# Performance work log

Measured on AMD Instinct MI355X. Metric: run time of the kernel, lower is better.

## Reference

```python
import jax, jax.numpy as jnp
import numpy as np

DEPTH = 18                     # levels 0..17 of a complete binary tree
N = 2 ** DEPTH - 1             # 262143 nodes, node n's children are 2n+1, 2n+2


def setup_inputs() -> dict:
    key = jax.random.key(0)
    ks = jax.random.split(key, 9)
    V, X, H, C = 32000, 128, 128, 5
    s = 0.05  # weight scale to keep activations in a sane range
    return {
        "x_ids": jax.random.randint(ks[0], (N,), 0, V),
        "mask": jax.random.randint(ks[1], (N,), 0, 2),
        "emb_table": jax.random.normal(ks[2], (V, X), jnp.float32),
        "W_iou": jax.random.normal(ks[3], (X, 3 * H), jnp.float32) * s,
        "U_iou": jax.random.normal(ks[4], (H, 3 * H), jnp.float32) * s,
        "b_iou": jnp.zeros((3 * H,), jnp.float32),
        "W_f": jax.random.normal(ks[5], (X, H), jnp.float32) * s,
        "U_f": jax.random.normal(ks[6], (H, H), jnp.float32) * s,
        "b_f": jnp.zeros((H,), jnp.float32),
        "W_out": jax.random.normal(ks[7], (H, C), jnp.float32) * s,
        "b_out": jnp.zeros((C,), jnp.float32),
    }


def reference(x_ids, mask, emb_table, W_iou, U_iou, b_iou, W_f, U_f, b_f, W_out, b_out):
    H = U_f.shape[0]
    # input_module: embeds = Embedding(x * mask)
    embeds = emb_table[x_ids * mask]                    # [N, X]
    # cell_module.precompute_input_values: per-node input projections
    x_iou = embeds @ W_iou + b_iou                      # [N, 3H]
    x_f = embeds @ W_f + b_f                            # [N, H]

    levels_h = [None] * DEPTH
    levels_c = [None] * DEPTH
    # dgl.prop_nodes_topo: leaves -> root, one synchronized level at a time
    for d in range(DEPTH - 1, -1, -1):
        s0, n = 2 ** d - 1, 2 ** d                      # level-d node range [s0, s0+n)
        iou = x_iou[s0:s0 + n]
        if d < DEPTH - 1:
            # children of level-d node s0+i are contiguous at level d+1: 2i, 2i+1
            h_ch = levels_h[d + 1].reshape(n, 2, H)
            c_ch = levels_c[d + 1].reshape(n, 2, H)
            iou = iou + h_ch.sum(axis=1) @ U_iou        # child-sum of h
            f = jax.nn.sigmoid(x_f[s0:s0 + n][:, None, :] + h_ch @ U_f)  # [n,2,H]
            fc = (f * c_ch).sum(axis=1)
        else:
            fc = jnp.zeros((n, H), iou.dtype)
        i, o, u = jnp.split(iou, 3, axis=-1)
        c = jax.nn.sigmoid(i) * jnp.tanh(u) + fc
        h = jax.nn.sigmoid(o) * jnp.tanh(c)
        levels_h[d] = h
        levels_c[d] = c

    h_all = jnp.concatenate(levels_h, axis=0)           # [N, H], node-index order
    # output_module: per-node linear readout
    return h_all @ W_out + b_out                        # [N, C]
```

## Files before the change

kernel.cpp:

```cpp
#include <hip/hip_runtime.h>

#define DEPTH 18
#define NN ((1 << DEPTH) - 1)

typedef __attribute__((ext_vector_type(8))) short short8;
typedef __attribute__((ext_vector_type(4))) float f32x4;

__device__ __forceinline__ float sigm_(float x) { return 1.f / (1.f + __expf(-x)); }
__device__ __forceinline__ float tanh_(float x) { float e = __expf(2.f * x); return 1.f - 2.f / (e + 1.f); }
__device__ __forceinline__ unsigned short f2bf(float f) {
    union { float f; unsigned int u; } v; v.f = f;
    unsigned int r = (v.u + 0x7fffu + ((v.u >> 16) & 1u)) >> 16;
    return (unsigned short)r;
}
__device__ __forceinline__ float bf2f(unsigned short h) {
    union { unsigned int u; float f; } v; v.u = ((unsigned int)h) << 16; return v.f;
}
__device__ __forceinline__ uint4 bfadd8(uint4 a, uint4 b) {
    const unsigned short* pa = (const unsigned short*)&a;
    const unsigned short* pb = (const unsigned short*)&b;
    uint4 o; unsigned short* po = (unsigned short*)&o;
    #pragma unroll
    for (int i = 0; i < 8; ++i) po[i] = f2bf(bf2f(pa[i]) + bf2f(pb[i]));
    return o;
}

__global__ void cvt_emb(const float* __restrict__ src, unsigned short* __restrict__ dst, int n4) {
    int i = blockIdx.x * 256 + threadIdx.x;
    if (i < n4) {
        float4 v = ((const float4*)src)[i];
        ushort4 o; o.x = f2bf(v.x); o.y = f2bf(v.y); o.z = f2bf(v.z); o.w = f2bf(v.w);
        ((ushort4*)dst)[i] = o;
    }
}

__global__ void build_bpack(const float* __restrict__ Wiou, const float* __restrict__ Uiou,
                            const float* __restrict__ Wf, const float* __restrict__ Uf,
                            unsigned short* __restrict__ pack) {
    int idx = blockIdx.x * 256 + threadIdx.x;
    int c = idx >> 14, r = idx & 16383, j = r >> 5, kl = r & 31;
    int k2 = c * 32 + kl;
    float v;
    if (j < 384) v = (k2 < 128) ? Wiou[k2 * 384 + j] : Uiou[(k2 - 128) * 384 + j];
    else { int jf = j - 384; v = (k2 < 128) ? Wf[k2 * 128 + jf] : Uf[(k2 - 128) * 128 + jf]; }
    pack[idx] = f2bf(v);
}

__global__ void build_woutT(const float* __restrict__ Wout, float* __restrict__ woutT) {
    int i = blockIdx.x * 256 + threadIdx.x;
    if (i < 640) { int c = i >> 7, k = i & 127; woutT[c * 132 + k] = Wout[k * 5 + c]; }
}

template<int HC>
__global__ __launch_bounds__(256, 2) void tree_level_mfma(
    const int* __restrict__ xids, const int* __restrict__ msk,
    const unsigned short* __restrict__ embB, const unsigned short* __restrict__ bpack,
    const float* __restrict__ biou, const float* __restrict__ bfv,
    const float* __restrict__ woutT, const float* __restrict__ bout,
    unsigned short* __restrict__ hB, float* __restrict__ c_ws, float* __restrict__ outp,
    int s0)
{
    __shared__ __align__(16) unsigned short A_s[16896];

    const int t  = threadIdx.x;
    const int g0 = s0 + blockIdx.x * 32;

    {
        const int m = t >> 3, seg = t & 7;
        const int g = g0 + m;
        const int ei = xids[g] * msk[g];
        const int j0 = seg * 2;
        const uint4* es = (const uint4*)(embB + (size_t)ei * 128 + seg * 16);
        uint4 e0 = es[0], e1 = es[1];
        *(uint4*)&A_s[j0 * 264 + m * 8]       = e0;
        *(uint4*)&A_s[(j0 + 1) * 264 + m * 8] = e1;
        if (HC) {
            const int gl = 2 * g + 1;
            const uint4* lp = (const uint4*)(hB + (size_t)gl * 128 + seg * 16);
            const uint4* rp = (const uint4*)(hB + (size_t)(gl + 1) * 128 + seg * 16);
            uint4 l0 = lp[0], l1 = lp[1];
            uint4 r0 = rp[0], r1 = rp[1];
            *(uint4*)&A_s[2 * 4224 + j0 * 264 + m * 8]       = l0;
            *(uint4*)&A_s[2 * 4224 + (j0 + 1) * 264 + m * 8] = l1;
            *(uint4*)&A_s[3 * 4224 + j0 * 264 + m * 8]       = r0;
            *(uint4*)&A_s[3 * 4224 + (j0 + 1) * 264 + m * 8] = r1;
            uint4 s0v = bfadd8(l0, r0), s1v = bfadd8(l1, r1);
            *(uint4*)&A_s[4224 + j0 * 264 + m * 8]       = s0v;
            *(uint4*)&A_s[4224 + (j0 + 1) * 264 + m * 8] = s1v;
        }
    }
    __syncthreads();

    const int lane = t & 63, w = t >> 6;
    const int ln = lane & 15, q = lane >> 4;

    const unsigned short* bp = bpack + ln * 32 + q * 8;
    const unsigned short* ap = A_s + q * 264 + ln * 8;

#define BF(c, tile) (*(const short8*)(bp + (c) * 16384 + (tile) * 512))
#define AF(r, cc, rt) (*(const short8*)(ap + (r) * 4224 + (cc) * 1056 + (rt) * 128))
#define MM(acc, a, b) acc = __builtin_amdgcn_mfma_f32_16x16x32_bf16(a, b, acc, 0, 0, 0)

    f32x4 accI[2][2] = {}, accO[2][2] = {}, accU[2][2] = {}, accFl[2][2] = {}, accFr[2][2] = {};
    const int ti = 2 * w, to = 8 + 2 * w, tu = 16 + 2 * w, tf = 24 + 2 * w;

    #pragma unroll
    for (int c = 0; c < 4; ++c) {
        short8 bI0 = BF(c, ti), bI1 = BF(c, ti + 1);
        short8 bO0 = BF(c, to), bO1 = BF(c, to + 1);
        short8 bU0 = BF(c, tu), bU1 = BF(c, tu + 1);
        short8 aE0 = AF(0, c, 0), aE1 = AF(0, c, 1);
        MM(accI[0][0], aE0, bI0); MM(accI[0][1], aE0, bI1);
        MM(accI[1][0], aE1, bI0); MM(accI[1][1], aE1, bI1);
        MM(accO[0][0], aE0, bO0); MM(accO[0][1], aE0, bO1);
        MM(accO[1][0], aE1, bO0); MM(accO[1][1], aE1, bO1);
        MM(accU[0][0], aE0, bU0); MM(accU[0][1], aE0, bU1);
        MM(accU[1][0], aE1, bU0); MM(accU[1][1], aE1, bU1);
        if (HC) {
            short8 bF0 = BF(c, tf), bF1 = BF(c, tf + 1);
            MM(accFl[0][0], aE0, bF0); MM(accFl[0][1], aE0, bF1);
            MM(accFl[1][0], aE1, bF0); MM(accFl[1][1], aE1, bF1);
        }
    }
    if (HC) {
        #pragma unroll
        for (int rt = 0; rt < 2; ++rt)
            #pragma unroll
            for (int jt = 0; jt < 2; ++jt)
                accFr[rt][jt] = accFl[rt][jt];
        #pragma unroll
        for (int c = 0; c < 4; ++c) {
            short8 bI0 = BF(4 + c, ti), bI1 = BF(4 + c, ti + 1);
            short8 bO0 = BF(4 + c, to), bO1 = BF(4 + c, to + 1);
            short8 bU0 = BF(4 + c, tu), bU1 = BF(4 + c, tu + 1);
            short8 bF0 = BF(4 + c, tf), bF1 = BF(4 + c, tf + 1);
            short8 aH0 = AF(1, c, 0), aH1 = AF(1, c, 1);
            short8 aL0 = AF(2, c, 0), aL1 = AF(2, c, 1);
            short8 aR0 = AF(3, c, 0), aR1 = AF(3, c, 1);
            MM(accI[0][0], aH0, bI0); MM(accI[0][1], aH0, bI1);
            MM(accI[1][0], aH1, bI0); MM(accI[1][1], aH1, bI1);
            MM(accO[0][0], aH0, bO0); MM(accO[0][1], aH0, bO1);
            MM(accO[1][0], aH1, bO0); MM(accO[1][1], aH1, bO1);
            MM(accU[0][0], aH0, bU0); MM(accU[0][1], aH0, bU1);
            MM(accU[1][0], aH1, bU0); MM(accU[1][1], aH1, bU1);
            MM(accFl[0][0], aL0, bF0); MM(accFl[0][1], aL0, bF1);
            MM(accFl[1][0], aL1, bF0); MM(accFl[1][1], aL1, bF1);
            MM(accFr[0][0], aR0, bF0); MM(accFr[0][1], aR0, bF1);
            MM(accFr[1][0], aR1, bF0); MM(accFr[1][1], aR1, bF1);
        }
    }
#undef BF
#undef AF

    __syncthreads();
    float* h_s = (float*)A_s;

    #pragma unroll
    for (int rt = 0; rt < 2; ++rt) {
        #pragma unroll
        for (int jt = 0; jt < 2; ++jt) {
            const int col = w * 32 + jt * 16 + ln;
            const float bib = biou[col], bob = biou[128 + col], bub = biou[256 + col];
            const float bfb = bfv[col];
            #pragma unroll
            for (int r = 0; r < 4; ++r) {
                const int row = rt * 16 + q * 4 + r;
                const int g = g0 + row;
                const float iv = accI[rt][jt][r] + bib;
                const float ov = accO[rt][jt][r] + bob;
                const float uv = accU[rt][jt][r] + bub;
                float fc = 0.f;
                if (HC) {
                    const float cl = c_ws[(size_t)(2 * g + 1) * 128 + col];
                    const float cr = c_ws[(size_t)(2 * g + 2) * 128 + col];
                    const float fl = sigm_(accFl[rt][jt][r] + bfb);
                    const float fr = sigm_(accFr[rt][jt][r] + bfb);
                    fc = fl * cl + fr * cr;
                }
                const float cc = sigm_(iv) * tanh_(uv) + fc;
                const float hh = sigm_(ov) * tanh_(cc);
                c_ws[(size_t)g * 128 + col] = cc;
                hB[(size_t)g * 128 + col] = f2bf(hh);
                h_s[row * 136 + col] = hh;
            }
        }
    }
    __syncthreads();
    if (t < 160) {
        const int n = t / 5, cc5 = t - 5 * n;
        float acc = bout[cc5];
        #pragma unroll 4
        for (int k4 = 0; k4 < 32; ++k4) {
            const float4 hv = *(const float4*)&h_s[n * 136 + k4 * 4];
            const float4 wv = *(const float4*)&woutT[cc5 * 132 + k4 * 4];
            acc += hv.x * wv.x + hv.y * wv.y + hv.z * wv.z + hv.w * wv.w;
        }
        outp[(size_t)(g0 + n) * 5 + cc5] = acc;
    }
}

#define MM(acc, a, b) acc = __builtin_amdgcn_mfma_f32_16x16x32_bf16(a, b, acc, 0, 0, 0)
__global__ __launch_bounds__(256) void tree_subtree(
    const int* __restrict__ xids, const int* __restrict__ msk,
    const unsigned short* __restrict__ embB, const unsigned short* __restrict__ bpack,
    const float* __restrict__ biou, const float* __restrict__ bfv,
    const float* __restrict__ Wout, const float* __restrict__ bout,
    unsigned short* __restrict__ hB, float* __restrict__ c_ws, float* __restrict__ outp,
    int dTop, int dBot)
{
    __shared__ __align__(16) unsigned short A_s[6144];
    __shared__ __align__(16) float cbuf[2][16][128];
    __shared__ __align__(16) float wout_s[640];

    const int t = threadIdx.x, b = blockIdx.x;
    const int lane = t & 63, w = t >> 6;
    const int ln = lane & 15, q = lane >> 4;

    if (t < 160) ((float4*)wout_s)[t] = ((const float4*)Wout)[t];

    const int col0 = w * 32 + ln, col1 = col0 + 16;
    const float bib0 = biou[col0], bob0 = biou[128 + col0], bub0 = biou[256 + col0], bfb0 = bfv[col0];
    const float bib1 = biou[col1], bob1 = biou[128 + col1], bub1 = biou[256 + col1], bfb1 = bfv[col1];

    const unsigned short* bp = bpack + ln * 32 + q * 8;
    const unsigned short* ap = A_s + (q * 16 + ln) * 8;
    const int ti = 2 * w, to = 8 + 2 * w, tu = 16 + 2 * w, tf = 24 + 2 * w;

    for (int d = dTop; d >= dBot; --d) {
        const int nd = 1 << (d - dBot);
        const int g0 = ((1 << d) - 1) + (b << (d - dBot));
        const int par = (dTop - d) & 1;

        if (t < 128) {
            const int m = t >> 3, seg = t & 7;
            const int g = g0 + m;
            const int ei = xids[g] * msk[g];
            const uint4* es = (const uint4*)(embB + (size_t)ei * 128 + seg * 16);
            uint4 e0 = es[0], e1 = es[1];
            const int cc = seg >> 1, q0 = (seg & 1) * 2;
            *(uint4*)&A_s[cc * 512 + (q0 * 16 + m) * 8]       = e0;
            *(uint4*)&A_s[cc * 512 + ((q0 + 1) * 16 + m) * 8] = e1;
        }
        if (d == dTop) {
            const int row = t >> 3, sg = t & 7;
            const int child = 2 * g0 + 1 + row;
            const uint4* hp = (const uint4*)(hB + (size_t)child * 128 + sg * 16);
            uint4 h0 = hp[0], h1 = hp[1];
            const int reg = 1 + (row & 1), mm = row >> 1;
            const int cc = sg >> 1, q0 = (sg & 1) * 2;
            *(uint4*)&A_s[reg * 2048 + cc * 512 + (q0 * 16 + mm) * 8]       = h0;
            *(uint4*)&A_s[reg * 2048 + cc * 512 + ((q0 + 1) * 16 + mm) * 8] = h1;
        }
        __syncthreads();

        f32x4 accI[2] = {}, accO[2] = {}, accU[2] = {}, accFl[2] = {}, accFr[2] = {};
#define BF1(c, tile) (*(const short8*)(bp + (c) * 16384 + (tile) * 512))
#define AF1(r, c) (*(const short8*)(ap + (r) * 2048 + (c) * 512))
        #pragma unroll
        for (int c = 0; c < 4; ++c) {
            short8 aE = AF1(0, c);
            MM(accI[0], aE, BF1(c, ti)); MM(accI[1], aE, BF1(c, ti + 1));
            MM(accO[0], aE, BF1(c, to)); MM(accO[1], aE, BF1(c, to + 1));
            MM(accU[0], aE, BF1(c, tu)); MM(accU[1], aE, BF1(c, tu + 1));
            MM(accFl[0], aE, BF1(c, tf)); MM(accFl[1], aE, BF1(c, tf + 1));
        }
        accFr[0] = accFl[0]; accFr[1] = accFl[1];
        #pragma unroll
        for (int c = 0; c < 4; ++c) {
            short8 aL = AF1(1, c), aR = AF1(2, c);
            short8 bI0 = BF1(4 + c, ti), bI1 = BF1(4 + c, ti + 1);
            short8 bO0 = BF1(4 + c, to), bO1 = BF1(4 + c, to + 1);
            short8 bU0 = BF1(4 + c, tu), bU1 = BF1(4 + c, tu + 1);
            short8 bF0 = BF1(4 + c, tf), bF1 = BF1(4 + c, tf + 1);
            MM(accI[0], aL, bI0); MM(accI[0], aR, bI0);
            MM(accI[1], aL, bI1); MM(accI[1], aR, bI1);
            MM(accO[0], aL, bO0); MM(accO[0], aR, bO0);
            MM(accO[1], aL, bO1); MM(accO[1], aR, bO1);
            MM(accU[0], aL, bU0); MM(accU[0], aR, bU0);
            MM(accU[1], aL, bU1); MM(accU[1], aR, bU1);
            MM(accFl[0], aL, bF0); MM(accFl[1], aL, bF1);
            MM(accFr[0], aR, bF0); MM(accFr[1], aR, bF1);
        }
#undef BF1
#undef AF1
        __syncthreads();

        #pragma unroll
        for (int jt = 0; jt < 2; ++jt) {
            const int col = jt ? col1 : col0;
            const float bib = jt ? bib1 : bib0, bob = jt ? bob1 : bob0;
            const float bub = jt ? bub1 : bub0, bfb = jt ? bfb1 : bfb0;
            const f32x4 aI = accI[jt], aO = accO[jt], aU = accU[jt];
            const f32x4 aFl = accFl[jt], aFr = accFr[jt];
            #pragma unroll
            for (int r = 0; r < 4; ++r) {
                const int row = q * 4 + r;
                const int g = g0 + row;
                float cl, cr;
                if (d == dTop) {
                    cl = c_ws[(size_t)(2 * g + 1) * 128 + col];
                    cr = c_ws[(size_t)(2 * g + 2) * 128 + col];
                } else {
                    cl = cbuf[1 - par][2 * row][col];
                    cr = cbuf[1 - par][2 * row + 1][col];
                }
                const float iv = aI[r] + bib;
                const float ov = aO[r] + bob;
                const float uv = aU[r] + bub;
                const float fl = sigm_(aFl[r] + bfb);
                const float fr = sigm_(aFr[r] + bfb);
                const float cc = sigm_(iv) * tanh_(uv) + fl * cl + fr * cr;
                const float hh = sigm_(ov) * tanh_(cc);
                cbuf[par][row][col] = cc;
                const unsigned short hb = f2bf(hh);
                const int reg = 1 + (row & 1), mm = row >> 1;
                A_s[reg * 2048 + (col >> 5) * 512 + ((((col >> 3) & 3) * 16) + mm) * 8 + (col & 7)] = hb;
                if (row < nd) {
                    c_ws[(size_t)g * 128 + col] = cc;
                    hB[(size_t)g * 128 + col] = hb;
                }
            }
        }
        __syncthreads();
        if (t < nd * 5) {
            const int n = t / 5, cc5 = t - 5 * n;
            const int reg = 1 + (n & 1), mm = n >> 1;
            float acc = bout[cc5];
            #pragma unroll 8
            for (int k = 0; k < 128; ++k) {
                const float hv = bf2f(A_s[reg * 2048 + (k >> 5) * 512 + ((((k >> 3) & 3) * 16) + mm) * 8 + (k & 7)]);
                acc += hv * wout_s[k * 5 + cc5];
            }
            outp[(size_t)(g0 + n) * 5 + cc5] = acc;
        }
        __syncthreads();
    }
}
#undef MM

extern "C" void kernel_launch(void* const* d_in, const int* in_sizes, int n_in,
                              void* d_out, int out_size, void* d_ws, size_t ws_size,
                              hipStream_t stream)
{
    (void)in_sizes; (void)n_in; (void)out_size; (void)ws_size;
    const int*   xids = (const int*)d_in[0];
    const int*   msk  = (const int*)d_in[1];
    const float* emb  = (const float*)d_in[2];
    const float* Wiou = (const float*)d_in[3];
    const float* Uiou = (const float*)d_in[4];
    const float* biou = (const float*)d_in[5];
    const float* Wf   = (const float*)d_in[6];
    const float* Uf   = (const float*)d_in[7];
    const float* bfv  = (const float*)d_in[8];
    const float* Wout = (const float*)d_in[9];
    const float* bout = (const float*)d_in[10];
    float* outp = (float*)d_out;

    unsigned short* embB  = (unsigned short*)d_ws;
    unsigned short* bpack = embB + (size_t)32000 * 128;
    unsigned short* hB    = bpack + 131072;
    float*          c_ws  = (float*)(hB + (size_t)NN * 128);
    float*          woutT = c_ws + (size_t)NN * 128;

    cvt_emb<<<dim3((32000 * 128 / 4 + 255) / 256), dim3(256), 0, stream>>>(emb, embB, 32000 * 128 / 4);
    build_bpack<<<dim3(131072 / 256), dim3(256), 0, stream>>>(Wiou, Uiou, Wf, Uf, bpack);
    build_woutT<<<dim3(3), dim3(256), 0, stream>>>(Wout, woutT);

    {
        const int d = DEPTH - 1, s0 = (1 << d) - 1;
        tree_level_mfma<0><<<dim3((1 << d) / 32), dim3(256), 0, stream>>>(
            xids, msk, embB, bpack, biou, bfv, woutT, bout, hB, c_ws, outp, s0);
    }
    for (int d = DEPTH - 2; d >= 10; --d) {
        const int s0 = (1 << d) - 1;
        tree_level_mfma<1><<<dim3((1 << d) / 32), dim3(256), 0, stream>>>(
            xids, msk, embB, bpack, biou, bfv, woutT, bout, hB, c_ws, outp, s0);
    }
    tree_subtree<<<dim3(32), dim3(256), 0, stream>>>(
        xids, msk, embB, bpack, biou, bfv, Wout, bout, hB, c_ws, outp, 9, 5);
    tree_subtree<<<dim3(1), dim3(256), 0, stream>>>(
        xids, msk, embB, bpack, biou, bfv, Wout, bout, hB, c_ws, outp, 4, 0);
}
```

Before: 406.0 us.

## Fuse all tree levels into one persistent cooperative kernel with grid syncs

Replaces the chain of per-level launches plus the weight-prep kernels with a single cooperative persistent kernel. It converts the embeddings and packs the weights, then walks levels 17..5 using grid-stride tiles separated by grid-wide barriers, and finishes the top 5 levels in one block. The 32-block subtree stage is replaced by per-level tiles down to level 5, so the small levels now go through grid syncs instead of separate launches. This removes launch overhead and idle gaps between the many small dependent levels. The cost is one grid barrier per level, less parallelism on the small levels, and an occupancy cap from the shared persistent layout. A fallback path with separate launches is kept.

```diff
diff --git a/kernel.cpp b/kernel.cpp
--- a/kernel.cpp
+++ b/kernel.cpp
@@ -1,4 +1,7 @@
 #include <hip/hip_runtime.h>
+#include <hip/hip_cooperative_groups.h>
+
+namespace cg = cooperative_groups;
 
 #define DEPTH 18
 #define NN ((1 << DEPTH) - 1)
@@ -25,46 +28,19 @@
     return o;
 }
 
-__global__ void cvt_emb(const float* __restrict__ src, unsigned short* __restrict__ dst, int n4) {
-    int i = blockIdx.x * 256 + threadIdx.x;
-    if (i < n4) {
-        float4 v = ((const float4*)src)[i];
-        ushort4 o; o.x = f2bf(v.x); o.y = f2bf(v.y); o.z = f2bf(v.z); o.w = f2bf(v.w);
-        ((ushort4*)dst)[i] = o;
-    }
-}
-
-__global__ void build_bpack(const float* __restrict__ Wiou, const float* __restrict__ Uiou,
-                            const float* __restrict__ Wf, const float* __restrict__ Uf,
-                            unsigned short* __restrict__ pack) {
-    int idx = blockIdx.x * 256 + threadIdx.x;
-    int c = idx >> 14, r = idx & 16383, j = r >> 5, kl = r & 31;
-    int k2 = c * 32 + kl;
-    float v;
-    if (j < 384) v = (k2 < 128) ? Wiou[k2 * 384 + j] : Uiou[(k2 - 128) * 384 + j];
-    else { int jf = j - 384; v = (k2 < 128) ? Wf[k2 * 128 + jf] : Uf[(k2 - 128) * 128 + jf]; }
-    pack[idx] = f2bf(v);
-}
-
-__global__ void build_woutT(const float* __restrict__ Wout, float* __restrict__ woutT) {
-    int i = blockIdx.x * 256 + threadIdx.x;
-    if (i < 640) { int c = i >> 7, k = i & 127; woutT[c * 132 + k] = Wout[k * 5 + c]; }
-}
+#define MM(acc, a, b) acc = __builtin_amdgcn_mfma_f32_16x16x32_bf16(a, b, acc, 0, 0, 0)
 
 template<int HC>
-__global__ __launch_bounds__(256, 2) void tree_level_mfma(
+__device__ __forceinline__ void level_tile(
+    unsigned short* __restrict__ A_s,
     const int* __restrict__ xids, const int* __restrict__ msk,
     const unsigned short* __restrict__ embB, const unsigned short* __restrict__ bpack,
     const float* __restrict__ biou, const float* __restrict__ bfv,
     const float* __restrict__ woutT, const float* __restrict__ bout,
     unsigned short* __restrict__ hB, float* __restrict__ c_ws, float* __restrict__ outp,
-    int s0)
-{
-    __shared__ __align__(16) unsigned short A_s[16896];
-
-    const int t  = threadIdx.x;
-    const int g0 = s0 + blockIdx.x * 32;
-
+    int g0)
+{
+    const int t = threadIdx.x;
     {
         const int m = t >> 3, seg = t & 7;
         const int g = g0 + m;
@@ -99,7 +75,6 @@
 
 #define BF(c, tile) (*(const short8*)(bp + (c) * 16384 + (tile) * 512))
 #define AF(r, cc, rt) (*(const short8*)(ap + (r) * 4224 + (cc) * 1056 + (rt) * 128))
-#define MM(acc, a, b) acc = __builtin_amdgcn_mfma_f32_16x16x32_bf16(a, b, acc, 0, 0, 0)
 
     f32x4 accI[2][2] = {}, accO[2][2] = {}, accU[2][2] = {}, accFl[2][2] = {}, accFr[2][2] = {};
     const int ti = 2 * w, to = 8 + 2 * w, tu = 16 + 2 * w, tf = 24 + 2 * w;
@@ -197,22 +172,22 @@
         }
         outp[(size_t)(g0 + n) * 5 + cc5] = acc;
     }
-}
-
-#define MM(acc, a, b) acc = __builtin_amdgcn_mfma_f32_16x16x32_bf16(a, b, acc, 0, 0, 0)
-__global__ __launch_bounds__(256) void tree_subtree(
+    __syncthreads();
+}
+
+__device__ __forceinline__ void subtree40(
+    unsigned short* __restrict__ A_s,
     const int* __restrict__ xids, const int* __restrict__ msk,
     const unsigned short* __restrict__ embB, const unsigned short* __restrict__ bpack,
     const float* __restrict__ biou, const float* __restrict__ bfv,
     const float* __restrict__ Wout, const float* __restrict__ bout,
-    unsigned short* __restrict__ hB, float* __restrict__ c_ws, float* __restrict__ outp,
-    int dTop, int dBot)
-{
-    __shared__ __align__(16) unsigned short A_s[6144];
-    __shared__ __align__(16) float cbuf[2][16][128];
-    __shared__ __align__(16) float wout_s[640];
-
-    const int t = threadIdx.x, b = blockIdx.x;
+    unsigned short* __restrict__ hB, float* __restrict__ c_ws, float* __restrict__ outp)
+{
+    unsigned short* A2 = A_s;
+    float* cbufp  = (float*)(A_s + 6144);
+    float* wout_s = (float*)(A_s + 14336);
+
+    const int t = threadIdx.x;
     const int lane = t & 63, w = t >> 6;
     const int ln = lane & 15, q = lane >> 4;
 
@@ -223,13 +198,13 @@
     const float bib1 = biou[col1], bob1 = biou[128 + col1], bub1 = biou[256 + col1], bfb1 = bfv[col1];
 
     const unsigned short* bp = bpack + ln * 32 + q * 8;
-    const unsigned short* ap = A_s + (q * 16 + ln) * 8;
+    const unsigned short* ap = A2 + (q * 16 + ln) * 8;
     const int ti = 2 * w, to = 8 + 2 * w, tu = 16 + 2 * w, tf = 24 + 2 * w;
 
-    for (int d = dTop; d >= dBot; --d) {
-        const int nd = 1 << (d - dBot);
-        const int g0 = ((1 << d) - 1) + (b << (d - dBot));
-        const int par = (dTop - d) & 1;
+    for (int d = 4; d >= 0; --d) {
+        const int nd = 1 << d;
+        const int g0 = (1 << d) - 1;
+        const int par = (4 - d) & 1;
 
         if (t < 128) {
             const int m = t >> 3, seg = t & 7;
@@ -238,18 +213,18 @@
             const uint4* es = (const uint4*)(embB + (size_t)ei * 128 + seg * 16);
             uint4 e0 = es[0], e1 = es[1];
             const int cc = seg >> 1, q0 = (seg & 1) * 2;
-            *(uint4*)&A_s[cc * 512 + (q0 * 16 + m) * 8]       = e0;
-            *(uint4*)&A_s[cc * 512 + ((q0 + 1) * 16 + m) * 8] = e1;
-        }
-        if (d == dTop) {
+            *(uint4*)&A2[cc * 512 + (q0 * 16 + m) * 8]       = e0;
+            *(uint4*)&A2[cc * 512 + ((q0 + 1) * 16 + m) * 8] = e1;
+        }
+        if (d == 4) {
             const int row = t >> 3, sg = t & 7;
             const int child = 2 * g0 + 1 + row;
             const uint4* hp = (const uint4*)(hB + (size_t)child * 128 + sg * 16);
             uint4 h0 = hp[0], h1 = hp[1];
-            const int reg = 1 + (row & 1), mm = row >> 1;
+            const int reg = 1 + (row & 1), mm2 = row >> 1;
             const int cc = sg >> 1, q0 = (sg & 1) * 2;
-            *(uint4*)&A_s[reg * 2048 + cc * 512 + (q0 * 16 + mm) * 8]       = h0;
-            *(uint4*)&A_s[reg * 2048 + cc * 512 + ((q0 + 1) * 16 + mm) * 8] = h1;
+            *(uint4*)&A2[reg * 2048 + cc * 512 + (q0 * 16 + mm2) * 8]       = h0;
+            *(uint4*)&A2[reg * 2048 + cc * 512 + ((q0 + 1) * 16 + mm2) * 8] = h1;
         }
         __syncthreads();
 
@@ -297,12 +272,12 @@
                 const int row = q * 4 + r;
                 const int g = g0 + row;
                 float cl, cr;
-                if (d == dTop) {
+                if (d == 4) {
                     cl = c_ws[(size_t)(2 * g + 1) * 128 + col];
                     cr = c_ws[(size_t)(2 * g + 2) * 128 + col];
                 } else {
-                    cl = cbuf[1 - par][2 * row][col];
-                    cr = cbuf[1 - par][2 * row + 1][col];
+                    cl = cbufp[(1 - par) * 2048 + (2 * row) * 128 + col];
+                    cr = cbufp[(1 - par) * 2048 + (2 * row + 1) * 128 + col];
                 }
                 const float iv = aI[r] + bib;
                 const float ov = aO[r] + bob;
@@ -311,10 +286,10 @@
                 const float fr = sigm_(aFr[r] + bfb);
                 const float cc = sigm_(iv) * tanh_(uv) + fl * cl + fr * cr;
                 const float hh = sigm_(ov) * tanh_(cc);
-                cbuf[par][row][col] = cc;
+                cbufp[par * 2048 + row * 128 + col] = cc;
                 const unsigned short hb = f2bf(hh);
-                const int reg = 1 + (row & 1), mm = row >> 1;
-                A_s[reg * 2048 + (col >> 5) * 512 + ((((col >> 3) & 3) * 16) + mm) * 8 + (col & 7)] = hb;
+                const int reg = 1 + (row & 1), mm2 = row >> 1;
+                A2[reg * 2048 + (col >> 5) * 512 + ((((col >> 3) & 3) * 16) + mm2) * 8 + (col & 7)] = hb;
                 if (row < nd) {
                     c_ws[(size_t)g * 128 + col] = cc;
                     hB[(size_t)g * 128 + col] = hb;
@@ -324,11 +299,11 @@
         __syncthreads();
         if (t < nd * 5) {
             const int n = t / 5, cc5 = t - 5 * n;
-            const int reg = 1 + (n & 1), mm = n >> 1;
+            const int reg = 1 + (n & 1), mm2 = n >> 1;
             float acc = bout[cc5];
             #pragma unroll 8
             for (int k = 0; k < 128; ++k) {
-                const float hv = bf2f(A_s[reg * 2048 + (k >> 5) * 512 + ((((k >> 3) & 3) * 16) + mm) * 8 + (k & 7)]);
+                const float hv = bf2f(A2[reg * 2048 + (k >> 5) * 512 + ((((k >> 3) & 3) * 16) + mm2) * 8 + (k & 7)]);
                 acc += hv * wout_s[k * 5 + cc5];
             }
             outp[(size_t)(g0 + n) * 5 + cc5] = acc;
@@ -336,7 +311,111 @@
         __syncthreads();
     }
 }
+
+__global__ __launch_bounds__(256) void tree_all(
+    const int* __restrict__ xids, const int* __restrict__ msk,
+    const float* __restrict__ emb,
+    const float* __restrict__ Wiou, const float* __restrict__ Uiou, const float* __restrict__ biou,
+    const float* __restrict__ Wf, const float* __restrict__ Uf, const float* __restrict__ bfv,
+    const float* __restrict__ Wout, const float* __restrict__ bout,
+    unsigned short* __restrict__ embB, unsigned short* __restrict__ bpack,
+    unsigned short* __restrict__ hB, float* __restrict__ c_ws,
+    float* __restrict__ woutT, float* __restrict__ outp)
+{
+    __shared__ __align__(16) unsigned short A_s[16896];
+    cg::grid_group gg = cg::this_grid();
+
+    const int t = threadIdx.x;
+    const int gid = blockIdx.x * 256 + t;
+    const int gstride = gridDim.x * 256;
+
+    for (int i = gid; i < 1024000; i += gstride) {
+        float4 v = ((const float4*)emb)[i];
+        ushort4 o; o.x = f2bf(v.x); o.y = f2bf(v.y); o.z = f2bf(v.z); o.w = f2bf(v.w);
+        ((ushort4*)embB)[i] = o;
+    }
+    for (int i = gid; i < 131072; i += gstride) {
+        int c = i >> 14, r = i & 16383, j = r >> 5, kl = r & 31;
+        int k2 = c * 32 + kl;
+        float v;
+        if (j < 384) v = (k2 < 128) ? Wiou[k2 * 384 + j] : Uiou[(k2 - 128) * 384 + j];
+        else { int jf = j - 384; v = (k2 < 128) ? Wf[k2 * 128 + jf] : Uf[(k2 - 128) * 128 + jf]; }
+        bpack[i] = f2bf(v);
+    }
+    if (blockIdx.x == 0)
+        for (int i = t; i < 640; i += 256) {
+            int c = i >> 7, k = i & 127;
+            woutT[c * 132 + k] = Wout[k * 5 + c];
+        }
+    __threadfence();
+    gg.sync();
+
+    for (int d = 17; d >= 5; --d) {
+        const int s0 = (1 << d) - 1;
+        const int nt = 1 << (d - 5);
+        if (d == 17) {
+            for (int tile = blockIdx.x; tile < nt; tile += gridDim.x)
+                level_tile<0>(A_s, xids, msk, embB, bpack, biou, bfv, woutT, bout,
+                              hB, c_ws, outp, s0 + tile * 32);
+        } else {
+            for (int tile = blockIdx.x; tile < nt; tile += gridDim.x)
+                level_tile<1>(A_s, xids, msk, embB, bpack, biou, bfv, woutT, bout,
+                              hB, c_ws, outp, s0 + tile * 32);
+        }
+        __threadfence();
+        gg.sync();
+    }
+
+    if (blockIdx.x == 0)
+        subtree40(A_s, xids, msk, embB, bpack, biou, bfv, Wout, bout, hB, c_ws, outp);
+}
 #undef MM
+
+__global__ void cvt_emb(const float* __restrict__ src, unsigned short* __restrict__ dst, int n4) {
+    int i = blockIdx.x * 256 + threadIdx.x;
+    if (i < n4) {
+        float4 v = ((const float4*)src)[i];
+        ushort4 o; o.x = f2bf(v.x); o.y = f2bf(v.y); o.z = f2bf(v.z); o.w = f2bf(v.w);
+        ((ushort4*)dst)[i] = o;
+    }
+}
+__global__ void build_bpack(const float* __restrict__ Wiou, const float* __restrict__ Uiou,
+                            const float* __restrict__ Wf, const float* __restrict__ Uf,
+                            unsigned short* __restrict__ pack) {
+    int idx = blockIdx.x * 256 + threadIdx.x;
+    int c = idx >> 14, r = idx & 16383, j = r >> 5, kl = r & 31;
+    int k2 = c * 32 + kl;
+    float v;
+    if (j < 384) v = (k2 < 128) ? Wiou[k2 * 384 + j] : Uiou[(k2 - 128) * 384 + j];
+    else { int jf = j - 384; v = (k2 < 128) ? Wf[k2 * 128 + jf] : Uf[(k2 - 128) * 128 + jf]; }
+    pack[idx] = f2bf(v);
+}
+__global__ void build_woutT(const float* __restrict__ Wout, float* __restrict__ woutT) {
+    int i = blockIdx.x * 256 + threadIdx.x;
+    if (i < 640) { int c = i >> 7, k = i & 127; woutT[c * 132 + k] = Wout[k * 5 + c]; }
+}
+template<int HC>
+__global__ __launch_bounds__(256, 2) void k_level(
+    const int* __restrict__ xids, const int* __restrict__ msk,
+    const unsigned short* __restrict__ embB, const unsigned short* __restrict__ bpack,
+    const float* __restrict__ biou, const float* __restrict__ bfv,
+    const float* __restrict__ woutT, const float* __restrict__ bout,
+    unsigned short* __restrict__ hB, float* __restrict__ c_ws, float* __restrict__ outp, int s0)
+{
+    __shared__ __align__(16) unsigned short A_s[16896];
+    level_tile<HC>(A_s, xids, msk, embB, bpack, biou, bfv, woutT, bout,
+                   hB, c_ws, outp, s0 + blockIdx.x * 32);
+}
+__global__ __launch_bounds__(256) void k_sub40(
+    const int* __restrict__ xids, const int* __restrict__ msk,
+    const unsigned short* __restrict__ embB, const unsigned short* __restrict__ bpack,
+    const float* __restrict__ biou, const float* __restrict__ bfv,
+    const float* __restrict__ Wout, const float* __restrict__ bout,
+    unsigned short* __restrict__ hB, float* __restrict__ c_ws, float* __restrict__ outp)
+{
+    __shared__ __align__(16) unsigned short A_s[16896];
+    subtree40(A_s, xids, msk, embB, bpack, biou, bfv, Wout, bout, hB, c_ws, outp);
+}
 
 extern "C" void kernel_launch(void* const* d_in, const int* in_sizes, int n_in,
                               void* d_out, int out_size, void* d_ws, size_t ws_size,
@@ -362,22 +441,54 @@
     float*          c_ws  = (float*)(hB + (size_t)NN * 128);
     float*          woutT = c_ws + (size_t)NN * 128;
 
-    cvt_emb<<<dim3((32000 * 128 / 4 + 255) / 256), dim3(256), 0, stream>>>(emb, embB, 32000 * 128 / 4);
-    build_bpack<<<dim3(131072 / 256), dim3(256), 0, stream>>>(Wiou, Uiou, Wf, Uf, bpack);
-    build_woutT<<<dim3(3), dim3(256), 0, stream>>>(Wout, woutT);
-
-    {
-        const int d = DEPTH - 1, s0 = (1 << d) - 1;
-        tree_level_mfma<0><<<dim3((1 << d) / 32), dim3(256), 0, stream>>>(
-            xids, msk, embB, bpack, biou, bfv, woutT, bout, hB, c_ws, outp, s0);
-    }
-    for (int d = DEPTH - 2; d >= 10; --d) {
-        const int s0 = (1 << d) - 1;
-        tree_level_mfma<1><<<dim3((1 << d) / 32), dim3(256), 0, stream>>>(
-            xids, msk, embB, bpack, biou, bfv, woutT, bout, hB, c_ws, outp, s0);
-    }
-    tree_subtree<<<dim3(32), dim3(256), 0, stream>>>(
-        xids, msk, embB, bpack, biou, bfv, Wout, bout, hB, c_ws, outp, 9, 5);
-    tree_subtree<<<dim3(1), dim3(256), 0, stream>>>(
-        xids, msk, embB, bpack, biou, bfv, Wout, bout, hB, c_ws, outp, 4, 0);
-}
+    int dev = 0; hipGetDevice(&dev);
+    int numCU = 256;
+    hipDeviceGetAttribute(&numCU, hipDeviceAttributeMultiprocessorCount, dev);
+    int coopOK = 0;
+    hipDeviceGetAttribute(&coopOK, hipDeviceAttributeCooperativeLaunch, dev);
+    int maxB = 0;
+    hipOccupancyMaxActiveBlocksPerMultiprocessor(&maxB, (const void*)tree_all, 256, 0);
+    if (maxB < 1) maxB = 1;
+    if (maxB > 4) maxB = 4;
+
+    void* params[] = {
+        (void*)&xids, (void*)&msk, (void*)&emb,
+        (void*)&Wiou, (void*)&Uiou, (void*)&biou,
+        (void*)&Wf, (void*)&Uf, (void*)&bfv,
+        (void*)&Wout, (void*)&bout,
+        (void*)&embB, (void*)&bpack, (void*)&hB, (void*)&c_ws,
+        (void*)&woutT, (void*)&outp
+    };
+
+    hipError_t err = hipErrorUnknown;
+    if (coopOK) {
+        int tries[4] = { numCU * maxB, 768, 512, 256 };
+        for (int i = 0; i < 4; ++i) {
+            int g = tries[i];
+            if (g < 256) g = 256;
+            if (i > 0 && tries[i] >= tries[0]) continue;
+            err = hipLaunchCooperativeKernel((const void*)tree_all, dim3(g), dim3(256),
+                                             params, 0, stream);
+            if (err == hipSuccess) break;
+            (void)hipGetLastError();
+        }
+    }
+
+    if (err != hipSuccess) {
+        cvt_emb<<<dim3((32000 * 128 / 4 + 255) / 256), dim3(256), 0, stream>>>(emb, embB, 32000 * 128 / 4);
+        build_bpack<<<dim3(131072 / 256), dim3(256), 0, stream>>>(Wiou, Uiou, Wf, Uf, bpack);
+        build_woutT<<<dim3(3), dim3(256), 0, stream>>>(Wout, woutT);
+        {
+            const int d = 17, s0 = (1 << d) - 1;
+            k_level<0><<<dim3(1 << (d - 5)), dim3(256), 0, stream>>>(
+                xids, msk, embB, bpack, biou, bfv, woutT, bout, hB, c_ws, outp, s0);
+        }
+        for (int d = 16; d >= 5; --d) {
+            const int s0 = (1 << d) - 1;
+            k_level<1><<<dim3(1 << (d - 5)), dim3(256), 0, stream>>>(
+                xids, msk, embB, bpack, biou, bfv, woutT, bout, hB, c_ws, outp, s0);
+        }
+        k_sub40<<<dim3(1), dim3(256), 0, stream>>>(
+            xids, msk, embB, bpack, biou, bfv, Wout, bout, hB, c_ws, outp);
+    }
+}
```

Result: slower. 1.225 ms (+201.7%).

## Merge prep kernels and run tree levels 14-10 in one subtree kernel

Applied to the files above, without the earlier changes.

Combines the three weight and embedding conversion kernels into one grid-stride prep kernel. Levels 14 through 10, previously one launch per level, now run inside a single tree_subtree launch of 1024 blocks, each owning a 32-leaf subtree and keeping cell state in shared memory between levels. This cuts kernel launches and inter-level global round trips. The cost is that upper levels inside each block use only a fraction of the block's threads, leaving lanes idle.

```diff
diff --git a/kernel.cpp b/kernel.cpp
--- a/kernel.cpp
+++ b/kernel.cpp
@@ -25,30 +25,29 @@
     return o;
 }
 
-__global__ void cvt_emb(const float* __restrict__ src, unsigned short* __restrict__ dst, int n4) {
-    int i = blockIdx.x * 256 + threadIdx.x;
-    if (i < n4) {
-        float4 v = ((const float4*)src)[i];
+__global__ void prep_all(const float* __restrict__ emb,
+                         const float* __restrict__ Wiou, const float* __restrict__ Uiou,
+                         const float* __restrict__ Wf, const float* __restrict__ Uf,
+                         const float* __restrict__ Wout,
+                         unsigned short* __restrict__ embB, unsigned short* __restrict__ bpack,
+                         float* __restrict__ woutT)
+{
+    const int gid = blockIdx.x * 256 + threadIdx.x;
+    const int gstride = gridDim.x * 256;
+    for (int i = gid; i < 1024000; i += gstride) {
+        float4 v = ((const float4*)emb)[i];
         ushort4 o; o.x = f2bf(v.x); o.y = f2bf(v.y); o.z = f2bf(v.z); o.w = f2bf(v.w);
-        ((ushort4*)dst)[i] = o;
-    }
-}
-
-__global__ void build_bpack(const float* __restrict__ Wiou, const float* __restrict__ Uiou,
-                            const float* __restrict__ Wf, const float* __restrict__ Uf,
-                            unsigned short* __restrict__ pack) {
-    int idx = blockIdx.x * 256 + threadIdx.x;
-    int c = idx >> 14, r = idx & 16383, j = r >> 5, kl = r & 31;
-    int k2 = c * 32 + kl;
-    float v;
-    if (j < 384) v = (k2 < 128) ? Wiou[k2 * 384 + j] : Uiou[(k2 - 128) * 384 + j];
-    else { int jf = j - 384; v = (k2 < 128) ? Wf[k2 * 128 + jf] : Uf[(k2 - 128) * 128 + jf]; }
-    pack[idx] = f2bf(v);
-}
-
-__global__ void build_woutT(const float* __restrict__ Wout, float* __restrict__ woutT) {
-    int i = blockIdx.x * 256 + threadIdx.x;
-    if (i < 640) { int c = i >> 7, k = i & 127; woutT[c * 132 + k] = Wout[k * 5 + c]; }
+        ((ushort4*)embB)[i] = o;
+    }
+    for (int i = gid; i < 131072; i += gstride) {
+        int c = i >> 14, r = i & 16383, j = r >> 5, kl = r & 31;
+        int k2 = c * 32 + kl;
+        float v;
+        if (j < 384) v = (k2 < 128) ? Wiou[k2 * 384 + j] : Uiou[(k2 - 128) * 384 + j];
+        else { int jf = j - 384; v = (k2 < 128) ? Wf[k2 * 128 + jf] : Uf[(k2 - 128) * 128 + jf]; }
+        bpack[i] = f2bf(v);
+    }
+    if (gid < 640) { int c = gid >> 7, k = gid & 127; woutT[c * 132 + k] = Wout[k * 5 + c]; }
 }
 
 template<int HC>
@@ -246,10 +245,10 @@
             const int child = 2 * g0 + 1 + row;
             const uint4* hp = (const uint4*)(hB + (size_t)child * 128 + sg * 16);
             uint4 h0 = hp[0], h1 = hp[1];
-            const int reg = 1 + (row & 1), mm = row >> 1;
+            const int reg = 1 + (row & 1), mm2 = row >> 1;
             const int cc = sg >> 1, q0 = (sg & 1) * 2;
-            *(uint4*)&A_s[reg * 2048 + cc * 512 + (q0 * 16 + mm) * 8]       = h0;
-            *(uint4*)&A_s[reg * 2048 + cc * 512 + ((q0 + 1) * 16 + mm) * 8] = h1;
+            *(uint4*)&A_s[reg * 2048 + cc * 512 + (q0 * 16 + mm2) * 8]       = h0;
+            *(uint4*)&A_s[reg * 2048 + cc * 512 + ((q0 + 1) * 16 + mm2) * 8] = h1;
         }
         __syncthreads();
 
@@ -313,8 +312,8 @@
                 const float hh = sigm_(ov) * tanh_(cc);
                 cbuf[par][row][col] = cc;
                 const unsigned short hb = f2bf(hh);
-                const int reg = 1 + (row & 1), mm = row >> 1;
-                A_s[reg * 2048 + (col >> 5) * 512 + ((((col >> 3) & 3) * 16) + mm) * 8 + (col & 7)] = hb;
+                const int reg = 1 + (row & 1), mm2 = row >> 1;
+                A_s[reg * 2048 + (col >> 5) * 512 + ((((col >> 3) & 3) * 16) + mm2) * 8 + (col & 7)] = hb;
                 if (row < nd) {
                     c_ws[(size_t)g * 128 + col] = cc;
                     hB[(size_t)g * 128 + col] = hb;
@@ -324,11 +323,11 @@
         __syncthreads();
         if (t < nd * 5) {
             const int n = t / 5, cc5 = t - 5 * n;
-            const int reg = 1 + (n & 1), mm = n >> 1;
+            const int reg = 1 + (n & 1), mm2 = n >> 1;
             float acc = bout[cc5];
             #pragma unroll 8
             for (int k = 0; k < 128; ++k) {
-                const float hv = bf2f(A_s[reg * 2048 + (k >> 5) * 512 + ((((k >> 3) & 3) * 16) + mm) * 8 + (k & 7)]);
+                const float hv = bf2f(A_s[reg * 2048 + (k >> 5) * 512 + ((((k >> 3) & 3) * 16) + mm2) * 8 + (k & 7)]);
                 acc += hv * wout_s[k * 5 + cc5];
             }
             outp[(size_t)(g0 + n) * 5 + cc5] = acc;
@@ -362,20 +361,20 @@
     float*          c_ws  = (float*)(hB + (size_t)NN * 128);
     float*          woutT = c_ws + (size_t)NN * 128;
 
-    cvt_emb<<<dim3((32000 * 128 / 4 + 255) / 256), dim3(256), 0, stream>>>(emb, embB, 32000 * 128 / 4);
-    build_bpack<<<dim3(131072 / 256), dim3(256), 0, stream>>>(Wiou, Uiou, Wf, Uf, bpack);
-    build_woutT<<<dim3(3), dim3(256), 0, stream>>>(Wout, woutT);
-
+    prep_all<<<dim3(1024), dim3(256), 0, stream>>>(emb, Wiou, Uiou, Wf, Uf, Wout,
+                                                   embB, bpack, woutT);
     {
-        const int d = DEPTH - 1, s0 = (1 << d) - 1;
-        tree_level_mfma<0><<<dim3((1 << d) / 32), dim3(256), 0, stream>>>(
+        const int d = 17, s0 = (1 << d) - 1;
+        tree_level_mfma<0><<<dim3(1 << (d - 5)), dim3(256), 0, stream>>>(
             xids, msk, embB, bpack, biou, bfv, woutT, bout, hB, c_ws, outp, s0);
     }
-    for (int d = DEPTH - 2; d >= 10; --d) {
+    for (int d = 16; d >= 15; --d) {
         const int s0 = (1 << d) - 1;
-        tree_level_mfma<1><<<dim3((1 << d) / 32), dim3(256), 0, stream>>>(
+        tree_level_mfma<1><<<dim3(1 << (d - 5)), dim3(256), 0, stream>>>(
             xids, msk, embB, bpack, biou, bfv, woutT, bout, hB, c_ws, outp, s0);
     }
+    tree_subtree<<<dim3(1024), dim3(256), 0, stream>>>(
+        xids, msk, embB, bpack, biou, bfv, Wout, bout, hB, c_ws, outp, 14, 10);
     tree_subtree<<<dim3(32), dim3(256), 0, stream>>>(
         xids, msk, embB, bpack, biou, bfv, Wout, bout, hB, c_ws, outp, 9, 5);
     tree_subtree<<<dim3(1), dim3(256), 0, stream>>>(
```

New measurement: 465.8 us. +14.7%, slower.
